# Kernel optimization log

Measured on AMD Instinct MI355X. Metric: run time of the kernel, lower is better.

## Reference

```python
import jax, jax.numpy as jnp
import numpy as np

D_MODEL = 768
NUM_HEADS = 12
D_HEAD = D_MODEL // NUM_HEADS


def setup_inputs() -> dict:
    key = jax.random.key(0)
    ks = jax.random.split(key, 11)
    B, S = 2, 2048
    scale = 1.0 / np.sqrt(D_MODEL)
    inp = {
        "query": jax.random.normal(ks[0], (B, S, D_MODEL), dtype=jnp.float32),
        "key": jax.random.normal(ks[1], (B, S, D_MODEL), dtype=jnp.float32),
        "value": jax.random.normal(ks[2], (B, S, D_MODEL), dtype=jnp.float32),
        "W_q": jax.random.normal(ks[3], (D_MODEL, D_MODEL), dtype=jnp.float32) * scale,
        "b_q": jnp.zeros((D_MODEL,), dtype=jnp.float32),
        "W_k": jax.random.normal(ks[4], (D_MODEL, D_MODEL), dtype=jnp.float32) * scale,
        "b_k": jnp.zeros((D_MODEL,), dtype=jnp.float32),
        "W_v": jax.random.normal(ks[5], (D_MODEL, D_MODEL), dtype=jnp.float32) * scale,
        "b_v": jnp.zeros((D_MODEL,), dtype=jnp.float32),
        "W_o": jax.random.normal(ks[6], (D_MODEL, D_MODEL), dtype=jnp.float32) * scale,
        "b_o": jnp.zeros((D_MODEL,), dtype=jnp.float32),
    }
    return inp


def _split_heads(x):
    # [B, S, D] -> [B, H, S, Dh]
    B, S, _ = x.shape
    return x.reshape(B, S, NUM_HEADS, D_HEAD).transpose(0, 2, 1, 3)


def reference(query, key, value, W_q, b_q, W_k, b_k, W_v, b_v, W_o, b_o):
    q = _split_heads(query @ W_q.T + b_q)   # [B,H,S,Dh]
    k = _split_heads(key @ W_k.T + b_k)
    v = _split_heads(value @ W_v.T + b_v)
    scores = jnp.einsum('bhqd,bhkd->bhqk', q, k) / np.sqrt(D_HEAD).astype(np.float32)
    attn = jax.nn.softmax(scores, axis=-1)  # [B,H,S,S]
    out = jnp.einsum('bhqk,bhkd->bhqd', attn, v)
    B, H, S, Dh = out.shape
    out = out.transpose(0, 2, 1, 3).reshape(B, S, D_MODEL)
    out = out @ W_o.T + b_o
    return out, attn
```

## Files before the change

### kernel.cpp

```cpp
#include <hip/hip_runtime.h>
#include <hip/hip_bf16.h>
#include <stdint.h>

#define B_ 2
#define S_ 2048
#define D_ 768
#define H_ 12
#define DH_ 64
#define M_ (B_ * S_)

typedef __hip_bfloat16 bf16_t;
typedef __attribute__((ext_vector_type(8))) short bf16x8;
typedef __attribute__((ext_vector_type(4))) float f32x4;

__device__ __forceinline__ void async_cp16(const void* g, void* lds) {
  __builtin_amdgcn_global_load_lds(
      (__attribute__((address_space(1))) void*)g,
      (__attribute__((address_space(3))) void*)lds, 16, 0, 0);
}

__global__ __launch_bounds__(256) void cvt_kernel(
    const float* __restrict__ s0, const float* __restrict__ s1,
    const float* __restrict__ s2, const float* __restrict__ s3,
    const float* __restrict__ s4, const float* __restrict__ s5,
    const float* __restrict__ s6,
    bf16_t* __restrict__ d0, bf16_t* __restrict__ d1, bf16_t* __restrict__ d2,
    bf16_t* __restrict__ d3, bf16_t* __restrict__ d4, bf16_t* __restrict__ d5,
    bf16_t* __restrict__ d6) {
  const int NX = 786432;
  const int NW = 147456;
  int idx = blockIdx.x * 256 + threadIdx.x;
  const float* s; bf16_t* d; int l;
  if      (idx < NX)            { s = s0; d = d0; l = idx; }
  else if (idx < 2 * NX)        { s = s1; d = d1; l = idx - NX; }
  else if (idx < 3 * NX)        { s = s2; d = d2; l = idx - 2 * NX; }
  else if (idx < 3 * NX + NW)   { s = s3; d = d3; l = idx - 3 * NX; }
  else if (idx < 3 * NX + 2*NW) { s = s4; d = d4; l = idx - (3 * NX + NW); }
  else if (idx < 3 * NX + 3*NW) { s = s5; d = d5; l = idx - (3 * NX + 2 * NW); }
  else                          { s = s6; d = d6; l = idx - (3 * NX + 3 * NW); }
  float4 f = ((const float4*)s)[l];
  union { bf16_t h[4]; uint64_t u; } pk;
  pk.h[0] = __float2bfloat16(f.x); pk.h[1] = __float2bfloat16(f.y);
  pk.h[2] = __float2bfloat16(f.z); pk.h[3] = __float2bfloat16(f.w);
  ((uint64_t*)d)[l] = pk.u;
}

__device__ __forceinline__ void gemm_core(
    const bf16_t* __restrict__ A, const bf16_t* __restrict__ W,
    bf16_t* sA, bf16_t* sB, int m0, int n0, f32x4 acc[4][4]) {
  const int tid = threadIdx.x;
  const int wave = tid >> 6, lane = tid & 63;
  const int quad = lane >> 4, col = lane & 15;
  const int wm = wave >> 1, wn = wave & 1;

  for (int kt = 0; kt < 768; kt += 64) {
    __syncthreads();
#pragma unroll
    for (int r2 = 0; r2 < 4; ++r2) {
      int cbase = r2 * 256 + wave * 64;
      int c = cbase + lane;
      int row = c >> 3, cpos = c & 7, csrc = cpos ^ (row & 7);
      async_cp16(A + (size_t)(m0 + row) * 768 + kt + csrc * 8, (char*)sA + cbase * 16);
      async_cp16(W + (size_t)(n0 + row) * 768 + kt + csrc * 8, (char*)sB + cbase * 16);
    }
    __syncthreads();
#pragma unroll
    for (int ks = 0; ks < 2; ++ks) {
      const int cl = ks * 4 + quad;
      bf16x8 af[4], bf8[4];
#pragma unroll
      for (int i = 0; i < 4; ++i) {
        int m = wm * 64 + i * 16 + col;
        af[i] = *(const bf16x8*)((const char*)sA + m * 128 + ((cl ^ (m & 7)) * 16));
      }
#pragma unroll
      for (int j = 0; j < 4; ++j) {
        int n = wn * 64 + j * 16 + col;
        bf8[j] = *(const bf16x8*)((const char*)sB + n * 128 + ((cl ^ (n & 7)) * 16));
      }
#pragma unroll
      for (int i = 0; i < 4; ++i)
#pragma unroll
        for (int j = 0; j < 4; ++j)
          acc[i][j] = __builtin_amdgcn_mfma_f32_16x16x32_bf16(af[i], bf8[j], acc[i][j], 0, 0, 0);
    }
  }
}

__global__ __launch_bounds__(256, 2) void qkv_gemm_kernel(
    const bf16_t* __restrict__ xq, const bf16_t* __restrict__ xk, const bf16_t* __restrict__ xv,
    const bf16_t* __restrict__ wq, const bf16_t* __restrict__ wk, const bf16_t* __restrict__ wv,
    const float* __restrict__ bq, const float* __restrict__ bk, const float* __restrict__ bv,
    bf16_t* __restrict__ Qb, bf16_t* __restrict__ Kb, bf16_t* __restrict__ Vt) {
  __shared__ bf16_t sA[128 * 64];
  __shared__ bf16_t sB[128 * 64];
  const int z = blockIdx.z;
  const bf16_t* A = (z == 0) ? xq : (z == 1) ? xk : xv;
  const bf16_t* W = (z == 0) ? wq : (z == 1) ? wk : wv;
  const float* bias = (z == 0) ? bq : (z == 1) ? bk : bv;
  const int m0 = blockIdx.y * 128, n0 = blockIdx.x * 128;
  f32x4 acc[4][4] = {};
  gemm_core(A, W, sA, sB, m0, n0, acc);

  const int tid = threadIdx.x;
  const int wave = tid >> 6, lane = tid & 63;
  const int quad = lane >> 4, col = lane & 15;
  const int wm = wave >> 1, wn = wave & 1;
  float bv4[4];
#pragma unroll
  for (int j = 0; j < 4; ++j) bv4[j] = bias[n0 + wn * 64 + j * 16 + col];

  if (z == 2) {
#pragma unroll
    for (int i = 0; i < 4; ++i)
#pragma unroll
      for (int j = 0; j < 4; ++j) {
        union { bf16_t h[4]; uint64_t u; } pk;
#pragma unroll
        for (int r = 0; r < 4; ++r) pk.h[r] = __float2bfloat16(acc[i][j][r] + bv4[j]);
        int sbase = m0 + wm * 64 + i * 16 + quad * 4;
        int b = sbase >> 11, s = sbase & 2047;
        int ng = n0 + wn * 64 + j * 16 + col;
        int h = ng >> 6, d = ng & 63;
        *(uint64_t*)(Vt + (((size_t)(b * H_ + h)) * DH_ + d) * S_ + s) = pk.u;
      }
  } else {
    const float scale = (z == 0) ? 0.125f : 1.0f;
    bf16_t* dst = (z == 0) ? Qb : Kb;
#pragma unroll
    for (int i = 0; i < 4; ++i)
#pragma unroll
      for (int j = 0; j < 4; ++j)
#pragma unroll
        for (int r = 0; r < 4; ++r) {
          int mg = m0 + wm * 64 + i * 16 + quad * 4 + r;
          int ng = n0 + wn * 64 + j * 16 + col;
          int b = mg >> 11, s = mg & 2047;
          int h = ng >> 6, d = ng & 63;
          dst[(((size_t)(b * H_ + h)) * S_ + s) * DH_ + d] =
              __float2bfloat16((acc[i][j][r] + bv4[j]) * scale);
        }
  }
}

__global__ __launch_bounds__(256, 2) void o_gemm_kernel(
    const bf16_t* __restrict__ Ob, const bf16_t* __restrict__ wo,
    const float* __restrict__ bo, float* __restrict__ out) {
  __shared__ bf16_t sA[128 * 64];
  __shared__ bf16_t sB[128 * 64];
  const int m0 = blockIdx.y * 128, n0 = blockIdx.x * 128;
  f32x4 acc[4][4] = {};
  gemm_core(Ob, wo, sA, sB, m0, n0, acc);
  const int tid = threadIdx.x;
  const int wave = tid >> 6, lane = tid & 63;
  const int quad = lane >> 4, col = lane & 15;
  const int wm = wave >> 1, wn = wave & 1;
  float bv4[4];
#pragma unroll
  for (int j = 0; j < 4; ++j) bv4[j] = bo[n0 + wn * 64 + j * 16 + col];
#pragma unroll
  for (int i = 0; i < 4; ++i)
#pragma unroll
    for (int j = 0; j < 4; ++j)
#pragma unroll
      for (int r = 0; r < 4; ++r) {
        int mg = m0 + wm * 64 + i * 16 + quad * 4 + r;
        int ng = n0 + wn * 64 + j * 16 + col;
        out[(size_t)mg * D_ + ng] = acc[i][j][r] + bv4[j];
      }
}

__global__ __launch_bounds__(256, 3) void attn_kernel(
    const bf16_t* __restrict__ Qb, const bf16_t* __restrict__ Kb,
    const bf16_t* __restrict__ Vt, float* __restrict__ attn,
    bf16_t* __restrict__ Ob) {
  const int tid = threadIdx.x;
  const int w = tid >> 6, lane = tid & 63;
  const int quad = lane >> 4, col = lane & 15;
  const int qt = blockIdx.x, bh = blockIdx.y;
  const int bb = bh / H_, hh = bh - bb * H_;
  const size_t headSD = (size_t)bh * (S_ * DH_);
  const size_t headDS = (size_t)bh * (DH_ * S_);
  const int q0 = qt * 64 + w * 16;

  bf16x8 aq[2];
#pragma unroll
  for (int ks = 0; ks < 2; ++ks)
    aq[ks] = *(const bf16x8*)(Qb + headSD +
                  (size_t)(q0 + col) * DH_ + ks * 32 + quad * 8);

  float rsum = 0.f;
  for (int t = 0; t < 64; ++t) {
    const int kg = t * 32;
    bf16x8 bk[2][2];
#pragma unroll
    for (int kk = 0; kk < 2; ++kk)
#pragma unroll
      for (int ks = 0; ks < 2; ++ks)
        bk[kk][ks] = *(const bf16x8*)(Kb + headSD +
                        (size_t)(kg + kk * 16 + col) * DH_ + ks * 32 + quad * 8);
    f32x4 sc[2] = {};
#pragma unroll
    for (int kk = 0; kk < 2; ++kk)
#pragma unroll
      for (int ks = 0; ks < 2; ++ks)
        sc[kk] = __builtin_amdgcn_mfma_f32_16x16x32_bf16(bk[kk][ks], aq[ks], sc[kk], 0, 0, 0);
#pragma unroll
    for (int kk = 0; kk < 2; ++kk)
#pragma unroll
      for (int r = 0; r < 4; ++r)
        rsum += __expf(sc[kk][r]);
  }
  rsum += __shfl_xor(rsum, 16, 64);
  rsum += __shfl_xor(rsum, 32, 64);
  const float li = 1.0f / rsum;

  f32x4 oacc[4] = {};
  float* aprow = attn + ((size_t)bh * S_ + (q0 + col)) * S_ + quad * 4;
  for (int t = 0; t < 64; ++t) {
    const int kg = t * 32;
    bf16x8 bk[2][2];
#pragma unroll
    for (int kk = 0; kk < 2; ++kk)
#pragma unroll
      for (int ks = 0; ks < 2; ++ks)
        bk[kk][ks] = *(const bf16x8*)(Kb + headSD +
                        (size_t)(kg + kk * 16 + col) * DH_ + ks * 32 + quad * 8);
    f32x4 sc[2] = {};
#pragma unroll
    for (int kk = 0; kk < 2; ++kk)
#pragma unroll
      for (int ks = 0; ks < 2; ++ks)
        sc[kk] = __builtin_amdgcn_mfma_f32_16x16x32_bf16(bk[kk][ks], aq[ks], sc[kk], 0, 0, 0);

    float pa[2][4];
#pragma unroll
    for (int kk = 0; kk < 2; ++kk)
#pragma unroll
      for (int r = 0; r < 4; ++r)
        pa[kk][r] = __expf(sc[kk][r]) * li;

    *(f32x4*)(aprow + kg)      = (f32x4){pa[0][0], pa[0][1], pa[0][2], pa[0][3]};
    *(f32x4*)(aprow + kg + 16) = (f32x4){pa[1][0], pa[1][1], pa[1][2], pa[1][3]};

    uint32_t dw[2][2];
#pragma unroll
    for (int kk = 0; kk < 2; ++kk)
#pragma unroll
      for (int p = 0; p < 2; ++p) {
        union { bf16_t h[2]; uint32_t u; } pk2;
        pk2.h[0] = __float2bfloat16(pa[kk][2 * p]);
        pk2.h[1] = __float2bfloat16(pa[kk][2 * p + 1]);
        dw[kk][p] = pk2.u;
      }

    const int s0 = ((2 * quad) & 3) * 16 + col;
    const int s1 = ((2 * quad + 1) & 3) * 16 + col;
    uint32_t a00 = (uint32_t)__shfl((int)dw[0][0], s0);
    uint32_t a01 = (uint32_t)__shfl((int)dw[0][1], s0);
    uint32_t a10 = (uint32_t)__shfl((int)dw[1][0], s0);
    uint32_t a11 = (uint32_t)__shfl((int)dw[1][1], s0);
    uint32_t b00 = (uint32_t)__shfl((int)dw[0][0], s1);
    uint32_t b01 = (uint32_t)__shfl((int)dw[0][1], s1);
    uint32_t b10 = (uint32_t)__shfl((int)dw[1][0], s1);
    uint32_t b11 = (uint32_t)__shfl((int)dw[1][1], s1);
    const bool hi2 = quad >= 2;
    union { uint32_t u[4]; bf16x8 v; } fr;
    fr.u[0] = hi2 ? a10 : a00;
    fr.u[1] = hi2 ? a11 : a01;
    fr.u[2] = hi2 ? b10 : b00;
    fr.u[3] = hi2 ? b11 : b01;

    bf16x8 bv[4];
#pragma unroll
    for (int j = 0; j < 4; ++j)
      bv[j] = *(const bf16x8*)(Vt + headDS +
                  (size_t)(16 * j + col) * S_ + kg + quad * 8);
#pragma unroll
    for (int j = 0; j < 4; ++j)
      oacc[j] = __builtin_amdgcn_mfma_f32_16x16x32_bf16(fr.v, bv[j], oacc[j], 0, 0, 0);
  }

#pragma unroll
  for (int j = 0; j < 4; ++j)
#pragma unroll
    for (int r = 0; r < 4; ++r)
      Ob[((size_t)bb * S_ + (q0 + quad * 4 + r)) * D_ + hh * 64 + 16 * j + col] =
          __float2bfloat16(oacc[j][r]);
}

extern "C" void kernel_launch(void* const* d_in, const int* in_sizes, int n_in,
                              void* d_out, int out_size, void* d_ws, size_t ws_size,
                              hipStream_t stream) {
  const float* q  = (const float*)d_in[0];
  const float* k  = (const float*)d_in[1];
  const float* v  = (const float*)d_in[2];
  const float* Wq = (const float*)d_in[3];
  const float* bq = (const float*)d_in[4];
  const float* Wk = (const float*)d_in[5];
  const float* bk = (const float*)d_in[6];
  const float* Wv = (const float*)d_in[7];
  const float* bv = (const float*)d_in[8];
  const float* Wo = (const float*)d_in[9];
  const float* bo = (const float*)d_in[10];
  char* ws = (char*)d_ws;
  bf16_t* xq = (bf16_t*)(ws + 0);
  bf16_t* xk = (bf16_t*)(ws + 6291456);
  bf16_t* xv = (bf16_t*)(ws + 12582912);
  bf16_t* wq = (bf16_t*)(ws + 18874368);
  bf16_t* wk = (bf16_t*)(ws + 20054016);
  bf16_t* wv = (bf16_t*)(ws + 21233664);
  bf16_t* wo = (bf16_t*)(ws + 22413312);
  bf16_t* Qb = (bf16_t*)(ws + 23592960);
  bf16_t* Kb = (bf16_t*)(ws + 29884416);
  bf16_t* Vt = (bf16_t*)(ws + 36175872);
  bf16_t* Ob = (bf16_t*)(ws + 42467328);
  float* out = (float*)d_out;
  float* attn = out + (size_t)M_ * D_;

  cvt_kernel<<<11520, 256, 0, stream>>>(q, k, v, Wq, Wk, Wv, Wo,
                                        xq, xk, xv, wq, wk, wv, wo);
  qkv_gemm_kernel<<<dim3(6, 32, 3), 256, 0, stream>>>(xq, xk, xv, wq, wk, wv,
                                                      bq, bk, bv, Qb, Kb, Vt);
  attn_kernel<<<dim3(32, 24), 256, 0, stream>>>(Qb, Kb, Vt, attn, Ob);
  o_gemm_kernel<<<dim3(6, 32), 256, 0, stream>>>(Ob, wo, bo, out);
}
```

Before: 727.8 us.

## Split attention key range across warps with LDS reduction and register prefetch

Each block now handles 16 queries instead of 64, and its four warps each cover a quarter of the key range. Row sums and partial outputs are combined through shared memory, and the grid grows fourfold. The aim is more blocks for better occupancy and shorter serial loops per warp. K fragments are also double-buffered in registers and V loads are issued earlier to hide memory latency. In exchange the kernel uses extra LDS, two block-wide syncs and a final reduction, and each block reloads Q for fewer rows.

Result: no change. 723.3 us (-0.6%).

```diff
diff --git a/kernel.cpp b/kernel.cpp
--- a/kernel.cpp
+++ b/kernel.cpp
@@ -174,6 +174,9 @@
     const bf16_t* __restrict__ Qb, const bf16_t* __restrict__ Kb,
     const bf16_t* __restrict__ Vt, float* __restrict__ attn,
     bf16_t* __restrict__ Ob) {
+  __shared__ float redS[4][16];
+  __shared__ float redO[4][16][64];
+
   const int tid = threadIdx.x;
   const int w = tid >> 6, lane = tid & 63;
   const int quad = lane >> 4, col = lane & 15;
@@ -181,7 +184,8 @@
   const int bb = bh / H_, hh = bh - bb * H_;
   const size_t headSD = (size_t)bh * (S_ * DH_);
   const size_t headDS = (size_t)bh * (DH_ * S_);
-  const int q0 = qt * 64 + w * 16;
+  const int q0 = qt * 16;
+  const int k0w = w * 512;
 
   bf16x8 aq[2];
 #pragma unroll
@@ -189,104 +193,146 @@
     aq[ks] = *(const bf16x8*)(Qb + headSD +
                   (size_t)(q0 + col) * DH_ + ks * 32 + quad * 8);
 
+  const bf16_t* Kbase = Kb + headSD;
+
   float rsum = 0.f;
-  for (int t = 0; t < 64; ++t) {
-    const int kg = t * 32;
-    bf16x8 bk[2][2];
+  {
+    bf16x8 bk[2][2], nk[2][2];
 #pragma unroll
     for (int kk = 0; kk < 2; ++kk)
 #pragma unroll
       for (int ks = 0; ks < 2; ++ks)
-        bk[kk][ks] = *(const bf16x8*)(Kb + headSD +
-                        (size_t)(kg + kk * 16 + col) * DH_ + ks * 32 + quad * 8);
-    f32x4 sc[2] = {};
-#pragma unroll
-    for (int kk = 0; kk < 2; ++kk)
-#pragma unroll
-      for (int ks = 0; ks < 2; ++ks)
-        sc[kk] = __builtin_amdgcn_mfma_f32_16x16x32_bf16(bk[kk][ks], aq[ks], sc[kk], 0, 0, 0);
-#pragma unroll
-    for (int kk = 0; kk < 2; ++kk)
-#pragma unroll
-      for (int r = 0; r < 4; ++r)
-        rsum += __expf(sc[kk][r]);
+        bk[kk][ks] = *(const bf16x8*)(Kbase +
+                        (size_t)(k0w + kk * 16 + col) * DH_ + ks * 32 + quad * 8);
+#pragma unroll 1
+    for (int t = 0; t < 16; ++t) {
+      const int kgn = k0w + ((t + 1) & 15) * 32;
+#pragma unroll
+      for (int kk = 0; kk < 2; ++kk)
+#pragma unroll
+        for (int ks = 0; ks < 2; ++ks)
+          nk[kk][ks] = *(const bf16x8*)(Kbase +
+                          (size_t)(kgn + kk * 16 + col) * DH_ + ks * 32 + quad * 8);
+      f32x4 sc[2] = {};
+#pragma unroll
+      for (int kk = 0; kk < 2; ++kk)
+#pragma unroll
+        for (int ks = 0; ks < 2; ++ks)
+          sc[kk] = __builtin_amdgcn_mfma_f32_16x16x32_bf16(bk[kk][ks], aq[ks], sc[kk], 0, 0, 0);
+#pragma unroll
+      for (int kk = 0; kk < 2; ++kk)
+#pragma unroll
+        for (int r = 0; r < 4; ++r)
+          rsum += __expf(sc[kk][r]);
+#pragma unroll
+      for (int kk = 0; kk < 2; ++kk)
+#pragma unroll
+        for (int ks = 0; ks < 2; ++ks)
+          bk[kk][ks] = nk[kk][ks];
+    }
   }
   rsum += __shfl_xor(rsum, 16, 64);
   rsum += __shfl_xor(rsum, 32, 64);
-  const float li = 1.0f / rsum;
+  if (lane < 16) redS[w][lane] = rsum;
+  __syncthreads();
+  const float li = 1.0f / (redS[0][col] + redS[1][col] + redS[2][col] + redS[3][col]);
 
   f32x4 oacc[4] = {};
   float* aprow = attn + ((size_t)bh * S_ + (q0 + col)) * S_ + quad * 4;
-  for (int t = 0; t < 64; ++t) {
-    const int kg = t * 32;
-    bf16x8 bk[2][2];
+  {
+    bf16x8 bk[2][2], nk[2][2];
 #pragma unroll
     for (int kk = 0; kk < 2; ++kk)
 #pragma unroll
       for (int ks = 0; ks < 2; ++ks)
-        bk[kk][ks] = *(const bf16x8*)(Kb + headSD +
-                        (size_t)(kg + kk * 16 + col) * DH_ + ks * 32 + quad * 8);
-    f32x4 sc[2] = {};
-#pragma unroll
-    for (int kk = 0; kk < 2; ++kk)
-#pragma unroll
-      for (int ks = 0; ks < 2; ++ks)
-        sc[kk] = __builtin_amdgcn_mfma_f32_16x16x32_bf16(bk[kk][ks], aq[ks], sc[kk], 0, 0, 0);
-
-    float pa[2][4];
-#pragma unroll
-    for (int kk = 0; kk < 2; ++kk)
-#pragma unroll
-      for (int r = 0; r < 4; ++r)
-        pa[kk][r] = __expf(sc[kk][r]) * li;
-
-    *(f32x4*)(aprow + kg)      = (f32x4){pa[0][0], pa[0][1], pa[0][2], pa[0][3]};
-    *(f32x4*)(aprow + kg + 16) = (f32x4){pa[1][0], pa[1][1], pa[1][2], pa[1][3]};
-
-    uint32_t dw[2][2];
-#pragma unroll
-    for (int kk = 0; kk < 2; ++kk)
-#pragma unroll
-      for (int p = 0; p < 2; ++p) {
-        union { bf16_t h[2]; uint32_t u; } pk2;
-        pk2.h[0] = __float2bfloat16(pa[kk][2 * p]);
-        pk2.h[1] = __float2bfloat16(pa[kk][2 * p + 1]);
-        dw[kk][p] = pk2.u;
-      }
-
-    const int s0 = ((2 * quad) & 3) * 16 + col;
-    const int s1 = ((2 * quad + 1) & 3) * 16 + col;
-    uint32_t a00 = (uint32_t)__shfl((int)dw[0][0], s0);
-    uint32_t a01 = (uint32_t)__shfl((int)dw[0][1], s0);
-    uint32_t a10 = (uint32_t)__shfl((int)dw[1][0], s0);
-    uint32_t a11 = (uint32_t)__shfl((int)dw[1][1], s0);
-    uint32_t b00 = (uint32_t)__shfl((int)dw[0][0], s1);
-    uint32_t b01 = (uint32_t)__shfl((int)dw[0][1], s1);
-    uint32_t b10 = (uint32_t)__shfl((int)dw[1][0], s1);
-    uint32_t b11 = (uint32_t)__shfl((int)dw[1][1], s1);
-    const bool hi2 = quad >= 2;
-    union { uint32_t u[4]; bf16x8 v; } fr;
-    fr.u[0] = hi2 ? a10 : a00;
-    fr.u[1] = hi2 ? a11 : a01;
-    fr.u[2] = hi2 ? b10 : b00;
-    fr.u[3] = hi2 ? b11 : b01;
-
-    bf16x8 bv[4];
-#pragma unroll
-    for (int j = 0; j < 4; ++j)
-      bv[j] = *(const bf16x8*)(Vt + headDS +
-                  (size_t)(16 * j + col) * S_ + kg + quad * 8);
-#pragma unroll
-    for (int j = 0; j < 4; ++j)
-      oacc[j] = __builtin_amdgcn_mfma_f32_16x16x32_bf16(fr.v, bv[j], oacc[j], 0, 0, 0);
+        bk[kk][ks] = *(const bf16x8*)(Kbase +
+                        (size_t)(k0w + kk * 16 + col) * DH_ + ks * 32 + quad * 8);
+#pragma unroll 1
+    for (int t = 0; t < 16; ++t) {
+      const int kg = k0w + t * 32;
+      const int kgn = k0w + ((t + 1) & 15) * 32;
+#pragma unroll
+      for (int kk = 0; kk < 2; ++kk)
+#pragma unroll
+        for (int ks = 0; ks < 2; ++ks)
+          nk[kk][ks] = *(const bf16x8*)(Kbase +
+                          (size_t)(kgn + kk * 16 + col) * DH_ + ks * 32 + quad * 8);
+      f32x4 sc[2] = {};
+#pragma unroll
+      for (int kk = 0; kk < 2; ++kk)
+#pragma unroll
+        for (int ks = 0; ks < 2; ++ks)
+          sc[kk] = __builtin_amdgcn_mfma_f32_16x16x32_bf16(bk[kk][ks], aq[ks], sc[kk], 0, 0, 0);
+
+      bf16x8 bv[4];
+#pragma unroll
+      for (int j = 0; j < 4; ++j)
+        bv[j] = *(const bf16x8*)(Vt + headDS +
+                    (size_t)(16 * j + col) * S_ + kg + quad * 8);
+
+      float pa[2][4];
+#pragma unroll
+      for (int kk = 0; kk < 2; ++kk)
+#pragma unroll
+        for (int r = 0; r < 4; ++r)
+          pa[kk][r] = __expf(sc[kk][r]) * li;
+
+      *(f32x4*)(aprow + kg)      = (f32x4){pa[0][0], pa[0][1], pa[0][2], pa[0][3]};
+      *(f32x4*)(aprow + kg + 16) = (f32x4){pa[1][0], pa[1][1], pa[1][2], pa[1][3]};
+
+      uint32_t dw[2][2];
+#pragma unroll
+      for (int kk = 0; kk < 2; ++kk)
+#pragma unroll
+        for (int p = 0; p < 2; ++p) {
+          union { bf16_t h[2]; uint32_t u; } pk2;
+          pk2.h[0] = __float2bfloat16(pa[kk][2 * p]);
+          pk2.h[1] = __float2bfloat16(pa[kk][2 * p + 1]);
+          dw[kk][p] = pk2.u;
+        }
+
+      const int s0 = ((2 * quad) & 3) * 16 + col;
+      const int s1 = ((2 * quad + 1) & 3) * 16 + col;
+      uint32_t a00 = (uint32_t)__shfl((int)dw[0][0], s0);
+      uint32_t a01 = (uint32_t)__shfl((int)dw[0][1], s0);
+      uint32_t a10 = (uint32_t)__shfl((int)dw[1][0], s0);
+      uint32_t a11 = (uint32_t)__shfl((int)dw[1][1], s0);
+      uint32_t b00 = (uint32_t)__shfl((int)dw[0][0], s1);
+      uint32_t b01 = (uint32_t)__shfl((int)dw[0][1], s1);
+      uint32_t b10 = (uint32_t)__shfl((int)dw[1][0], s1);
+      uint32_t b11 = (uint32_t)__shfl((int)dw[1][1], s1);
+      const bool hi2 = quad >= 2;
+      union { uint32_t u[4]; bf16x8 v; } fr;
+      fr.u[0] = hi2 ? a10 : a00;
+      fr.u[1] = hi2 ? a11 : a01;
+      fr.u[2] = hi2 ? b10 : b00;
+      fr.u[3] = hi2 ? b11 : b01;
+
+#pragma unroll
+      for (int j = 0; j < 4; ++j)
+        oacc[j] = __builtin_amdgcn_mfma_f32_16x16x32_bf16(fr.v, bv[j], oacc[j], 0, 0, 0);
+
+#pragma unroll
+      for (int kk = 0; kk < 2; ++kk)
+#pragma unroll
+        for (int ks = 0; ks < 2; ++ks)
+          bk[kk][ks] = nk[kk][ks];
+    }
   }
 
 #pragma unroll
   for (int j = 0; j < 4; ++j)
 #pragma unroll
     for (int r = 0; r < 4; ++r)
-      Ob[((size_t)bb * S_ + (q0 + quad * 4 + r)) * D_ + hh * 64 + 16 * j + col] =
-          __float2bfloat16(oacc[j][r]);
+      redO[w][quad * 4 + r][16 * j + col] = oacc[j][r];
+  __syncthreads();
+#pragma unroll
+  for (int r2 = 0; r2 < 4; ++r2) {
+    int q = w * 4 + r2;
+    float val = redO[0][q][lane] + redO[1][q][lane] +
+                redO[2][q][lane] + redO[3][q][lane];
+    Ob[((size_t)bb * S_ + (q0 + q)) * D_ + hh * 64 + lane] = __float2bfloat16(val);
+  }
 }
 
 extern "C" void kernel_launch(void* const* d_in, const int* in_sizes, int n_in,
@@ -322,6 +368,6 @@
                                         xq, xk, xv, wq, wk, wv, wo);
   qkv_gemm_kernel<<<dim3(6, 32, 3), 256, 0, stream>>>(xq, xk, xv, wq, wk, wv,
                                                       bq, bk, bv, Qb, Kb, Vt);
-  attn_kernel<<<dim3(32, 24), 256, 0, stream>>>(Qb, Kb, Vt, attn, Ob);
+  attn_kernel<<<dim3(128, 24), 256, 0, stream>>>(Qb, Kb, Vt, attn, Ob);
   o_gemm_kernel<<<dim3(6, 32), 256, 0, stream>>>(Ob, wo, bo, out);
 }
```
